# Kernel tuning notes

Measured on AMD Instinct MI355X. Metric: run time of the kernel, lower is better.

Reference implementation:

```python
import jax, jax.numpy as jnp
import numpy as np

DIM = 384
HEADS = 6
B, N = 4, 2048


def setup_inputs() -> dict:
    key = jax.random.key(0)
    ks = jax.random.split(key, 9)
    s = 0.02
    return {
        "x": jax.random.normal(ks[0], (B, N, DIM), dtype=jnp.float32),
        # weights stored [in, out] so y = x @ W + b (torch Linear transposed)
        "w_qkv": jax.random.normal(ks[1], (DIM, 3 * DIM), dtype=jnp.float32) * s,
        "b_qkv": jax.random.normal(ks[2], (3 * DIM,), dtype=jnp.float32) * s,
        "w_l": jax.random.normal(ks[3], (HEADS, HEADS), dtype=jnp.float32) * s,
        "b_l": jax.random.normal(ks[4], (HEADS,), dtype=jnp.float32) * s,
        "w_w": jax.random.normal(ks[5], (HEADS, HEADS), dtype=jnp.float32) * s,
        "b_w": jax.random.normal(ks[6], (HEADS,), dtype=jnp.float32) * s,
        "w_proj": jax.random.normal(ks[7], (DIM, DIM), dtype=jnp.float32) * s,
        "b_proj": jax.random.normal(ks[8], (DIM,), dtype=jnp.float32) * s,
    }


def reference(x, w_qkv, b_qkv, w_l, b_l, w_w, b_w, w_proj, b_proj):
    Bx, Nx, C = x.shape
    H = w_l.shape[0]
    d = C // H
    scale = d ** -0.5
    qkv = (x @ w_qkv + b_qkv).reshape(Bx, Nx, 3, H, d)
    q = jnp.transpose(qkv[:, :, 0], (0, 2, 1, 3)) * scale  # [B,H,N,d]
    k = jnp.transpose(qkv[:, :, 1], (0, 2, 1, 3))
    v = jnp.transpose(qkv[:, :, 2], (0, 2, 1, 3))
    attn = jnp.einsum("bhnd,bhmd->bhnm", q, k)  # [B,H,N,N]
    # talking-heads pre-softmax mix (linear over head axis)
    attn = jnp.einsum("bhnm,hg->bgnm", attn, w_l) + b_l[None, :, None, None]
    attn = jax.nn.softmax(attn, axis=-1)
    # talking-heads post-softmax mix
    attn = jnp.einsum("bhnm,hg->bgnm", attn, w_w) + b_w[None, :, None, None]
    out = jnp.einsum("bhnm,bhmd->bhnd", attn, v)  # [B,H,N,d]
    out = jnp.transpose(out, (0, 2, 1, 3)).reshape(Bx, Nx, C)
    return out @ w_proj + b_proj
```

## Files before the change

kernel.cpp:

```cpp
#include <hip/hip_runtime.h>

typedef unsigned short u16;
typedef unsigned int u32;
typedef float f32x4 __attribute__((ext_vector_type(4)));
typedef short bf16x8 __attribute__((ext_vector_type(8)));

#define MFMA16 __builtin_amdgcn_mfma_f32_16x16x32_bf16
#define LOG2E 1.44269504088896f

__device__ inline u16 f2bf(float f) {
    u32 u = __builtin_bit_cast(u32, f);
    u += 0x7FFFu + ((u >> 16) & 1u);
    return (u16)(u >> 16);
}
__device__ inline float bf2f(u16 v) {
    u32 u = ((u32)v) << 16;
    return __builtin_bit_cast(float, u);
}
__device__ inline u32 pack2(float a, float b) {
    return (u32)f2bf(a) | ((u32)f2bf(b) << 16);
}
__device__ inline f32x4 splat4(float x) { f32x4 r = {x, x, x, x}; return r; }
__device__ inline f32x4 fma4(f32x4 a, float b, f32x4 c) {
    return __builtin_elementwise_fma(a, splat4(b), c);
}
__device__ inline f32x4 mul4(f32x4 a, float b) { return a * splat4(b); }
__device__ inline float exp2b(float x) { return __builtin_amdgcn_exp2f(x); }
__device__ inline f32x4 exp2v(f32x4 x) {
    f32x4 r;
    r.x = exp2b(x.x); r.y = exp2b(x.y); r.z = exp2b(x.z); r.w = exp2b(x.w);
    return r;
}
__device__ inline float hmax4(f32x4 v) {
    return fmaxf(fmaxf(v.x, v.y), fmaxf(v.z, v.w));
}
__device__ inline float hsum4(f32x4 v) { return v.x + v.y + v.z + v.w; }
__device__ inline f32x4 vmax4(f32x4 a, f32x4 b) {
    f32x4 r;
    r.x = fmaxf(a.x, b.x); r.y = fmaxf(a.y, b.y);
    r.z = fmaxf(a.z, b.z); r.w = fmaxf(a.w, b.w);
    return r;
}

__global__ void cast_bf16_kernel(const float* __restrict__ in, u16* __restrict__ out, int n) {
    for (int i = blockIdx.x * blockDim.x + threadIdx.x; i < n; i += gridDim.x * blockDim.x)
        out[i] = f2bf(in[i]);
}

__global__ void transpose_w_kernel(const float* __restrict__ in, u16* __restrict__ out, int K, int C) {
    int c = blockIdx.x;
    for (int k = threadIdx.x; k < K; k += blockDim.x)
        out[c * K + k] = f2bf(in[k * C + c]);
}

__global__ __launch_bounds__(256) void qkv_gemm_kernel(
    const u16* __restrict__ xb, const u16* __restrict__ wT, const float* __restrict__ bias,
    u16* __restrict__ Qb, u16* __restrict__ Kb, u16* __restrict__ Vb) {
    int wave = threadIdx.x >> 6, lane = threadIdx.x & 63;
    int ln = lane & 15, gp = lane >> 4;
    int row0 = blockIdx.y * 64 + wave * 16;
    int col0 = blockIdx.x * 64;

    f32x4 acc[4];
#pragma unroll
    for (int cf = 0; cf < 4; cf++) acc[cf] = splat4(0.f);

    for (int k0 = 0; k0 < 384; k0 += 32) {
        bf16x8 a = *(const bf16x8*)&xb[(row0 + ln) * 384 + k0 + gp * 8];
#pragma unroll
        for (int cf = 0; cf < 4; cf++) {
            bf16x8 bb = *(const bf16x8*)&wT[(col0 + cf * 16 + ln) * 384 + k0 + gp * 8];
            acc[cf] = MFMA16(a, bb, acc[cf], 0, 0, 0);
        }
    }
#pragma unroll
    for (int cf = 0; cf < 4; cf++) {
        int col = col0 + cf * 16 + ln;
        int sec = (col >= 768) ? 2 : ((col >= 384) ? 1 : 0);
        int hc = col - sec * 384;
        int h = hc >> 6, dc = hc & 63;
        float bia = bias[col];
        u16* dst = (sec == 0) ? Qb : ((sec == 1) ? Kb : Vb);
        float scale = (sec == 0) ? 0.125f : 1.0f;
#pragma unroll
        for (int r = 0; r < 4; r++) {
            int row = row0 + gp * 4 + r;
            int b = row >> 11, n = row & 2047;
            float v = (acc[cf][r] + bia) * scale;
            dst[((b * 6 + h) * 2048 + n) * 64 + dc] = f2bf(v);
        }
    }
}

__global__ void vtrans_kernel(const u16* __restrict__ Vb, u16* __restrict__ Vt, float* __restrict__ sumV) {
    int blk = blockIdx.x;
    int nt = blk & 15, bh = blk >> 4;
    int n0 = nt * 128;
    __shared__ u16 t[64][136];
#pragma unroll
    for (int i = 0; i < 32; i++) {
        int idx = threadIdx.x + i * 256;
        int n = idx >> 6, dc = idx & 63;
        t[dc][n] = Vb[(bh * 2048 + n0 + n) * 64 + dc];
    }
    __syncthreads();
#pragma unroll
    for (int i = 0; i < 32; i++) {
        int idx = threadIdx.x + i * 256;
        int dc = idx >> 7, nl = idx & 127;
        Vt[(bh * 64 + dc) * 2048 + n0 + nl] = t[dc][nl];
    }
    if (threadIdx.x < 64) {
        float s = 0.f;
        for (int n = 0; n < 128; n++) s += bf2f(t[threadIdx.x][n]);
        atomicAdd(&sumV[bh * 64 + threadIdx.x], s);
    }
}

__global__ __launch_bounds__(128) void attn_stats_kernel(
    const u16* __restrict__ Qb, const u16* __restrict__ Kb,
    const float* __restrict__ w_l,
    float* __restrict__ sm, float* __restrict__ sl) {
    int wave = threadIdx.x >> 6, lane = threadIdx.x & 63;
    int ln = lane & 15, gp = lane >> 4;
    int b = blockIdx.x >> 6, nt = blockIdx.x & 63, c = blockIdx.y;
    int n0 = nt * 32 + wave * 16;

    float Wl[36];
#pragma unroll
    for (int i = 0; i < 36; i++) Wl[i] = w_l[i] * LOG2E;

    bf16x8 qf[6][2];
#pragma unroll
    for (int h = 0; h < 6; h++)
#pragma unroll
        for (int ks = 0; ks < 2; ks++)
            qf[h][ks] = *(const bf16x8*)&Qb[((b * 6 + h) * 2048 + n0 + ln) * 64 + ks * 32 + gp * 8];

    float mu[6], ll[6];
#pragma unroll
    for (int g = 0; g < 6; g++) { mu[g] = -1e30f; ll[g] = 0.f; }

    f32x4 S[6][2];
    for (int t = 0; t < 8; t++) {
        int m0 = c * 256 + t * 32;
#pragma unroll
        for (int h = 0; h < 6; h++) {
            const u16* kb = &Kb[((b * 6 + h) * 2048 + m0 + ln) * 64 + gp * 8];
#pragma unroll
            for (int mf = 0; mf < 2; mf++) {
                f32x4 a = splat4(0.f);
#pragma unroll
                for (int ks = 0; ks < 2; ks++) {
                    bf16x8 kf = *(const bf16x8*)(kb + mf * 1024 + ks * 32);
                    a = MFMA16(kf, qf[h][ks], a, 0, 0, 0);
                }
                S[h][mf] = a;
            }
        }
#pragma unroll
        for (int mf = 0; mf < 2; mf++) {
            f32x4 t0 = S[0][mf], t1 = S[1][mf], t2 = S[2][mf];
            f32x4 t3 = S[3][mf], t4 = S[4][mf], t5 = S[5][mf];
#pragma unroll
            for (int g = 0; g < 6; g++) {
                S[g][mf] = fma4(t0, Wl[g],
                           fma4(t1, Wl[6 + g],
                           fma4(t2, Wl[12 + g],
                           fma4(t3, Wl[18 + g],
                           fma4(t4, Wl[24 + g], mul4(t5, Wl[30 + g]))))));
            }
        }
#pragma unroll
        for (int g = 0; g < 6; g++) {
            f32x4 m4 = vmax4(S[g][0], S[g][1]);
            float tm = hmax4(m4);
            tm = fmaxf(tm, __shfl_xor(tm, 16));
            tm = fmaxf(tm, __shfl_xor(tm, 32));
            float nm = fmaxf(mu[g], tm);
            float corr = exp2b(mu[g] - nm);
            f32x4 s4 = exp2v(S[g][0] - splat4(nm)) + exp2v(S[g][1] - splat4(nm));
            float s = hsum4(s4);
            s += __shfl_xor(s, 16);
            s += __shfl_xor(s, 32);
            ll[g] = ll[g] * corr + s;
            mu[g] = nm;
        }
    }
    if (gp == 0) {
#pragma unroll
        for (int g = 0; g < 6; g++) {
            int idx = ((b * 6 + g) * 2048 + n0 + ln) * 8 + c;
            sm[idx] = mu[g];
            sl[idx] = ll[g];
        }
    }
}

__global__ __launch_bounds__(256) void stats_combine_kernel(
    const float* __restrict__ sm, const float* __restrict__ sl,
    float* __restrict__ MU, float* __restrict__ RL) {
    int i = blockIdx.x * 256 + threadIdx.x;
    float mu = -1e30f;
#pragma unroll
    for (int c = 0; c < 8; c++) mu = fmaxf(mu, sm[i * 8 + c]);
    float ll = 0.f;
#pragma unroll
    for (int c = 0; c < 8; c++) ll += sl[i * 8 + c] * exp2b(sm[i * 8 + c] - mu);
    MU[i] = mu;
    RL[i] = 1.f / ll;
}

__global__ __launch_bounds__(128) void attn_pv_kernel(
    const u16* __restrict__ Qb, const u16* __restrict__ Kb, const u16* __restrict__ Vt,
    const float* __restrict__ MU, const float* __restrict__ RL,
    const float* __restrict__ w_l, const float* __restrict__ w_w,
    float* __restrict__ O) {
    __shared__ __align__(16) u16 pbuf[2][6][16][40];

    int wave = threadIdx.x >> 6, lane = threadIdx.x & 63;
    int ln = lane & 15, gp = lane >> 4;
    int b = blockIdx.x >> 6, nt = blockIdx.x & 63, c = blockIdx.y;
    int n0 = nt * 32 + wave * 16;

    float Wl[36], Ww[36];
#pragma unroll
    for (int i = 0; i < 36; i++) Wl[i] = w_l[i] * LOG2E;
#pragma unroll
    for (int i = 0; i < 36; i++) Ww[i] = w_w[i];

    bf16x8 qf[6][2];
#pragma unroll
    for (int h = 0; h < 6; h++)
#pragma unroll
        for (int ks = 0; ks < 2; ks++)
            qf[h][ks] = *(const bf16x8*)&Qb[((b * 6 + h) * 2048 + n0 + ln) * 64 + ks * 32 + gp * 8];

    float mu[6], rl[6];
#pragma unroll
    for (int g = 0; g < 6; g++) {
        mu[g] = MU[(b * 6 + g) * 2048 + n0 + ln];
        rl[g] = RL[(b * 6 + g) * 2048 + n0 + ln];
    }

    f32x4 o[6][4];
#pragma unroll
    for (int g = 0; g < 6; g++)
#pragma unroll
        for (int dcf = 0; dcf < 4; dcf++) o[g][dcf] = splat4(0.f);

    f32x4 S[6][2];
    for (int t = 0; t < 8; t++) {
        int m0 = c * 256 + t * 32;
#pragma unroll
        for (int h = 0; h < 6; h++) {
            const u16* kb = &Kb[((b * 6 + h) * 2048 + m0 + ln) * 64 + gp * 8];
#pragma unroll
            for (int mf = 0; mf < 2; mf++) {
                f32x4 a = splat4(0.f);
#pragma unroll
                for (int ks = 0; ks < 2; ks++) {
                    bf16x8 kf = *(const bf16x8*)(kb + mf * 1024 + ks * 32);
                    a = MFMA16(kf, qf[h][ks], a, 0, 0, 0);
                }
                S[h][mf] = a;
            }
        }
#pragma unroll
        for (int mf = 0; mf < 2; mf++) {
            f32x4 t0 = S[0][mf], t1 = S[1][mf], t2 = S[2][mf];
            f32x4 t3 = S[3][mf], t4 = S[4][mf], t5 = S[5][mf];
#pragma unroll
            for (int g = 0; g < 6; g++) {
                S[g][mf] = fma4(t0, Wl[g],
                           fma4(t1, Wl[6 + g],
                           fma4(t2, Wl[12 + g],
                           fma4(t3, Wl[18 + g],
                           fma4(t4, Wl[24 + g], mul4(t5, Wl[30 + g]))))));
            }
        }
#pragma unroll
        for (int g = 0; g < 6; g++)
#pragma unroll
            for (int mf = 0; mf < 2; mf++)
                S[g][mf] = mul4(exp2v(S[g][mf] - splat4(mu[g])), rl[g]);
#pragma unroll
        for (int mf = 0; mf < 2; mf++) {
            f32x4 t0 = S[0][mf], t1 = S[1][mf], t2 = S[2][mf];
            f32x4 t3 = S[3][mf], t4 = S[4][mf], t5 = S[5][mf];
#pragma unroll
            for (int g = 0; g < 6; g++) {
                S[g][mf] = fma4(t0, Ww[g],
                           fma4(t1, Ww[6 + g],
                           fma4(t2, Ww[12 + g],
                           fma4(t3, Ww[18 + g],
                           fma4(t4, Ww[24 + g], mul4(t5, Ww[30 + g]))))));
            }
        }
#pragma unroll
        for (int g = 0; g < 6; g++)
#pragma unroll
            for (int mf = 0; mf < 2; mf++) {
                uint2 pk;
                pk.x = pack2(S[g][mf].x, S[g][mf].y);
                pk.y = pack2(S[g][mf].z, S[g][mf].w);
                *(uint2*)&pbuf[wave][g][ln][mf * 16 + gp * 4] = pk;
            }
#pragma unroll
        for (int g = 0; g < 6; g++) {
            bf16x8 pf = *(const bf16x8*)&pbuf[wave][g][ln][gp * 8];
#pragma unroll
            for (int dcf = 0; dcf < 4; dcf++) {
                bf16x8 vf = *(const bf16x8*)&Vt[((b * 6 + g) * 64 + dcf * 16 + ln) * 2048 + m0 + gp * 8];
                o[g][dcf] = MFMA16(vf, pf, o[g][dcf], 0, 0, 0);
            }
        }
    }
#pragma unroll
    for (int g = 0; g < 6; g++)
#pragma unroll
        for (int dcf = 0; dcf < 4; dcf++)
#pragma unroll
            for (int r = 0; r < 4; r++) {
                int dc = dcf * 16 + gp * 4 + r;
                atomicAdd(&O[((b * 6 + g) * 64 + dc) * 2048 + n0 + ln], o[g][dcf][r]);
            }
}

__global__ __launch_bounds__(256) void attn_epi_kernel(
    const float* __restrict__ O, const float* __restrict__ sumV,
    const float* __restrict__ b_w, u16* __restrict__ AO) {
    int bh = blockIdx.x;
    int b = bh / 6, g = bh % 6;
    int n0 = blockIdx.y * 64;
    __shared__ float tile[64][65];
    float bw = b_w[g];
#pragma unroll
    for (int i = 0; i < 16; i++) {
        int idx = threadIdx.x + i * 256;
        int dc = idx >> 6, n = idx & 63;
        tile[dc][n] = O[(bh * 64 + dc) * 2048 + n0 + n] + bw * sumV[bh * 64 + dc];
    }
    __syncthreads();
#pragma unroll
    for (int i = 0; i < 4; i++) {
        int idx = threadIdx.x + i * 256;
        int nl = idx >> 4, dq = idx & 15, dc = dq * 4;
        uint2 pk;
        pk.x = pack2(tile[dc][nl], tile[dc + 1][nl]);
        pk.y = pack2(tile[dc + 2][nl], tile[dc + 3][nl]);
        *(uint2*)&AO[(b * 2048 + n0 + nl) * 384 + g * 64 + dc] = pk;
    }
}

__global__ __launch_bounds__(256) void proj_gemm_kernel(
    const u16* __restrict__ AO, const u16* __restrict__ wT, const float* __restrict__ bias,
    float* __restrict__ out) {
    int wave = threadIdx.x >> 6, lane = threadIdx.x & 63;
    int ln = lane & 15, gp = lane >> 4;
    int row0 = blockIdx.y * 64 + wave * 16;
    int col0 = blockIdx.x * 64;

    f32x4 acc[4];
#pragma unroll
    for (int cf = 0; cf < 4; cf++) acc[cf] = splat4(0.f);

    for (int k0 = 0; k0 < 384; k0 += 32) {
        bf16x8 a = *(const bf16x8*)&AO[(row0 + ln) * 384 + k0 + gp * 8];
#pragma unroll
        for (int cf = 0; cf < 4; cf++) {
            bf16x8 bb = *(const bf16x8*)&wT[(col0 + cf * 16 + ln) * 384 + k0 + gp * 8];
            acc[cf] = MFMA16(a, bb, acc[cf], 0, 0, 0);
        }
    }
#pragma unroll
    for (int cf = 0; cf < 4; cf++) {
        int col = col0 + cf * 16 + ln;
        float bia = bias[col];
#pragma unroll
        for (int r = 0; r < 4; r++) {
            int row = row0 + gp * 4 + r;
            out[row * 384 + col] = acc[cf][r] + bia;
        }
    }
}

extern "C" void kernel_launch(void* const* d_in, const int* in_sizes, int n_in,
                              void* d_out, int out_size, void* d_ws, size_t ws_size,
                              hipStream_t stream) {
    const float* x      = (const float*)d_in[0];
    const float* w_qkv  = (const float*)d_in[1];
    const float* b_qkv  = (const float*)d_in[2];
    const float* w_l    = (const float*)d_in[3];
    const float* w_w    = (const float*)d_in[5];
    const float* b_w    = (const float*)d_in[6];
    const float* w_proj = (const float*)d_in[7];
    const float* b_proj = (const float*)d_in[8];

    char* base = (char*)d_ws;
    size_t off = 0;
    auto alloc = [&](size_t bytes) -> char* {
        char* p = base + off;
        off = (off + bytes + 255) & ~(size_t)255;
        return p;
    };
    u16* xb     = (u16*)alloc(8192 * 384 * 2);
    u16* wqkvT  = (u16*)alloc(1152 * 384 * 2);
    u16* wprojT = (u16*)alloc(384 * 384 * 2);
    u16* Qb     = (u16*)alloc(4 * 6 * 2048 * 64 * 2);
    u16* Kb     = (u16*)alloc(4 * 6 * 2048 * 64 * 2);
    u16* Vb     = (u16*)alloc(4 * 6 * 2048 * 64 * 2);
    u16* Vt     = (u16*)alloc(4 * 6 * 2048 * 64 * 2);
    float* sumV = (float*)alloc(4 * 6 * 64 * 4);
    u16* AO     = (u16*)alloc(8192 * 384 * 2);
    float* sm   = (float*)alloc(4 * 6 * 2048 * 8 * 4);
    float* sl   = (float*)alloc(4 * 6 * 2048 * 8 * 4);
    float* MU   = (float*)alloc(4 * 6 * 2048 * 4);
    float* RL   = (float*)alloc(4 * 6 * 2048 * 4);
    float* O    = (float*)alloc(4 * 6 * 64 * 2048 * 4);

    cast_bf16_kernel<<<2048, 256, 0, stream>>>(x, xb, 8192 * 384);
    transpose_w_kernel<<<1152, 128, 0, stream>>>(w_qkv, wqkvT, 384, 1152);
    transpose_w_kernel<<<384, 128, 0, stream>>>(w_proj, wprojT, 384, 384);
    qkv_gemm_kernel<<<dim3(18, 128), 256, 0, stream>>>(xb, wqkvT, b_qkv, Qb, Kb, Vb);
    hipMemsetAsync(sumV, 0, 4 * 6 * 64 * sizeof(float), stream);
    hipMemsetAsync(O, 0, (size_t)4 * 6 * 64 * 2048 * sizeof(float), stream);
    vtrans_kernel<<<384, 256, 0, stream>>>(Vb, Vt, sumV);
    attn_stats_kernel<<<dim3(256, 8), 128, 0, stream>>>(Qb, Kb, w_l, sm, sl);
    stats_combine_kernel<<<192, 256, 0, stream>>>(sm, sl, MU, RL);
    attn_pv_kernel<<<dim3(256, 8), 128, 0, stream>>>(Qb, Kb, Vt, MU, RL, w_l, w_w, O);
    attn_epi_kernel<<<dim3(24, 32), 256, 0, stream>>>(O, sumV, b_w, AO);
    proj_gemm_kernel<<<dim3(6, 128), 256, 0, stream>>>(AO, wprojT, b_proj, (float*)d_out);
}
```

Measured before the change: 738.7 us.

## Swizzle attention block order per XCD, keep head-mix weights in SGPRs, raise occupancy

Both attention kernels now take a flattened 1D grid. Block indices are decoded so that each XCD (blockIdx mod 8) handles a single batch and half of the key chunks, which should improve L2 reuse of K/V within each XCD. The talking-heads weights are forced into scalar registers with readfirstlane, freeing VGPRs. Launch bounds now request 3 blocks per CU. That may raise occupancy, but it risks spills if register pressure is still high.

```diff
diff --git a/kernel.cpp b/kernel.cpp
--- a/kernel.cpp
+++ b/kernel.cpp
@@ -40,6 +40,17 @@
     r.x = fmaxf(a.x, b.x); r.y = fmaxf(a.y, b.y);
     r.z = fmaxf(a.z, b.z); r.w = fmaxf(a.w, b.w);
     return r;
+}
+__device__ inline float sgpr(float v) {
+    return __builtin_bit_cast(float, __builtin_amdgcn_readfirstlane(__builtin_bit_cast(int, v)));
+}
+__device__ inline void decode_swz(int w, int& b, int& nt, int& c) {
+    int xcd = w & 7;
+    int idx = w >> 3;
+    b = xcd >> 1;
+    int sub = ((xcd & 1) << 8) | idx;
+    c = sub >> 6;
+    nt = sub & 63;
 }
 
 __global__ void cast_bf16_kernel(const float* __restrict__ in, u16* __restrict__ out, int n) {
@@ -117,18 +128,19 @@
     }
 }
 
-__global__ __launch_bounds__(128) void attn_stats_kernel(
+__global__ __launch_bounds__(128, 3) void attn_stats_kernel(
     const u16* __restrict__ Qb, const u16* __restrict__ Kb,
     const float* __restrict__ w_l,
     float* __restrict__ sm, float* __restrict__ sl) {
     int wave = threadIdx.x >> 6, lane = threadIdx.x & 63;
     int ln = lane & 15, gp = lane >> 4;
-    int b = blockIdx.x >> 6, nt = blockIdx.x & 63, c = blockIdx.y;
+    int b, nt, c;
+    decode_swz(blockIdx.x, b, nt, c);
     int n0 = nt * 32 + wave * 16;
 
     float Wl[36];
 #pragma unroll
-    for (int i = 0; i < 36; i++) Wl[i] = w_l[i] * LOG2E;
+    for (int i = 0; i < 36; i++) Wl[i] = sgpr(w_l[i] * LOG2E);
 
     bf16x8 qf[6][2];
 #pragma unroll
@@ -211,7 +223,7 @@
     RL[i] = 1.f / ll;
 }
 
-__global__ __launch_bounds__(128) void attn_pv_kernel(
+__global__ __launch_bounds__(128, 3) void attn_pv_kernel(
     const u16* __restrict__ Qb, const u16* __restrict__ Kb, const u16* __restrict__ Vt,
     const float* __restrict__ MU, const float* __restrict__ RL,
     const float* __restrict__ w_l, const float* __restrict__ w_w,
@@ -220,14 +232,15 @@
 
     int wave = threadIdx.x >> 6, lane = threadIdx.x & 63;
     int ln = lane & 15, gp = lane >> 4;
-    int b = blockIdx.x >> 6, nt = blockIdx.x & 63, c = blockIdx.y;
+    int b, nt, c;
+    decode_swz(blockIdx.x, b, nt, c);
     int n0 = nt * 32 + wave * 16;
 
     float Wl[36], Ww[36];
 #pragma unroll
-    for (int i = 0; i < 36; i++) Wl[i] = w_l[i] * LOG2E;
-#pragma unroll
-    for (int i = 0; i < 36; i++) Ww[i] = w_w[i];
+    for (int i = 0; i < 36; i++) Wl[i] = sgpr(w_l[i] * LOG2E);
+#pragma unroll
+    for (int i = 0; i < 36; i++) Ww[i] = sgpr(w_w[i]);
 
     bf16x8 qf[6][2];
 #pragma unroll
@@ -426,9 +439,9 @@
     hipMemsetAsync(sumV, 0, 4 * 6 * 64 * sizeof(float), stream);
     hipMemsetAsync(O, 0, (size_t)4 * 6 * 64 * 2048 * sizeof(float), stream);
     vtrans_kernel<<<384, 256, 0, stream>>>(Vb, Vt, sumV);
-    attn_stats_kernel<<<dim3(256, 8), 128, 0, stream>>>(Qb, Kb, w_l, sm, sl);
+    attn_stats_kernel<<<2048, 128, 0, stream>>>(Qb, Kb, w_l, sm, sl);
     stats_combine_kernel<<<192, 256, 0, stream>>>(sm, sl, MU, RL);
-    attn_pv_kernel<<<dim3(256, 8), 128, 0, stream>>>(Qb, Kb, Vt, MU, RL, w_l, w_w, O);
+    attn_pv_kernel<<<2048, 128, 0, stream>>>(Qb, Kb, Vt, MU, RL, w_l, w_w, O);
     attn_epi_kernel<<<dim3(24, 32), 256, 0, stream>>>(O, sumV, b_w, AO);
     proj_gemm_kernel<<<dim3(6, 128), 256, 0, stream>>>(AO, wprojT, b_proj, (float*)d_out);
 }
```

New measurement: 1.442 ms. 1.95x slower.
